# Kernel optimization log

Hardware: AMD Instinct MI355X
Metric: run time of the kernel (lower is better)

## Reference

```python
import jax, jax.numpy as jnp
import numpy as np

B, O, M, H, E = 32, 64, 128, 4, 64  # batch, num_obj, memory_len, heads, embed


def setup_inputs() -> dict:
    key = jax.random.key(0)
    ks = jax.random.split(key, 10)
    s = 1.0 / np.sqrt(E)
    return {
        "query": jax.random.normal(ks[0], (B, O, E), jnp.float32),
        "context": jax.random.normal(ks[1], (B, M, E), jnp.float32),
        "memory": jax.random.normal(ks[2], (B, M, E), jnp.float32),
        "W_ch": jax.random.normal(ks[3], (E, H * E), jnp.float32) * s,
        "b_ch": jax.random.normal(ks[4], (H * E,), jnp.float32) * s,
        "w_logit": jax.random.normal(ks[5], (E,), jnp.float32) * s,
        "b_logit": jax.random.normal(ks[6], (1,), jnp.float32) * s,
        "W_rh": jax.random.normal(ks[7], (H * E, E), jnp.float32) * (1.0 / np.sqrt(H * E)),
        "b_rh": jax.random.normal(ks[8], (E,), jnp.float32) * (1.0 / np.sqrt(H * E)),
        "temp": jnp.float32(1.0),
    }


def reference(query, context, memory, W_ch, b_ch, w_logit, b_logit, W_rh, b_rh, temp):
    # create heads: [B,O,E] -> [B,O,H,E]
    q = (query @ W_ch + b_ch).reshape(B, O, H, E)
    # broadcast add query heads and context over memory axis: [B,O,M,H,E]
    qc = jnp.tanh(context[:, None, :, None, :] + q[:, :, None, :, :])
    # logit projection -> [B,O,M,H]
    logits = jnp.einsum("bomhe,e->bomh", qc, w_logit) + b_logit[0]
    # softmax over memory axis (dim=2)
    probs = jax.nn.softmax(logits / temp, axis=2)
    # weighted sum of memory over M: [B,O,H,E]
    heads = jnp.einsum("bomh,bme->bohe", probs, memory)
    heads = jax.nn.leaky_relu(heads, negative_slope=0.01)
    out = heads.reshape(B, O, H * E) @ W_rh + b_rh
    return out
```

## Files before the change

### kernel.cpp

```cpp
#include <hip/hip_runtime.h>
#include <hip/hip_fp16.h>

#define B 32
#define O 64
#define M 128
#define H 4
#define E 64
#define SC 2.88539008177792681f
#define LOG2E 1.44269504088896341f

#if __has_builtin(__builtin_amdgcn_exp2f)
#define EXP2F(x) __builtin_amdgcn_exp2f(x)
#else
#define EXP2F(x) __exp2f(x)
#endif

__device__ __forceinline__ float rl(float v, int lane) {
    return __uint_as_float(__builtin_amdgcn_readlane(__float_as_uint(v), lane));
}
__device__ __forceinline__ unsigned pk2h(float a, float b) {
    return (unsigned)__half_as_ushort(__float2half_rn(a)) |
           ((unsigned)__half_as_ushort(__float2half_rn(b)) << 16);
}

__global__ __launch_bounds__(256) void prep_kernel(
    const float* __restrict__ query, const float* __restrict__ context,
    const float* __restrict__ memory, const float* __restrict__ W_ch,
    const float* __restrict__ b_ch,
    __half* __restrict__ ctx_Eh, __half* __restrict__ mem_T, float* __restrict__ q_E)
{
    __shared__ float s[128 * 68];
    const int t = threadIdx.x, blk = blockIdx.x;

    if (blk < 64) {
        const int b = blk & 31;
        const bool is_ctx = blk < 32;
        const int e = t >> 2, mb = (t & 3) * 32;
        const float* src = (is_ctx ? context : memory) + b * (M * E);
        #pragma unroll
        for (int i = 0; i < 8; ++i) {
            int idx = i * 1024 + t * 4;
            float4 v = *(const float4*)(src + idx);
            *(float4*)(&s[(idx >> 6) * 68 + (idx & 63)]) = v;
        }
        __syncthreads();
        if (is_ctx) {
            uint4* dst = (uint4*)(ctx_Eh + (size_t)b * (E * M) + e * M + mb);
            #pragma unroll
            for (int qd = 0; qd < 4; ++qd) {
                unsigned u[4];
                #pragma unroll
                for (int k = 0; k < 4; ++k) {
                    int m0 = mb + qd * 8 + 2 * k;
                    float ea = fminf(EXP2F(SC * s[m0 * 68 + e]), 60000.f);
                    float eb = fminf(EXP2F(SC * s[(m0 + 1) * 68 + e]), 60000.f);
                    u[k] = pk2h(ea, eb);
                }
                dst[qd] = make_uint4(u[0], u[1], u[2], u[3]);
            }
        } else {
            uint4* dst = (uint4*)(mem_T + (size_t)b * (E * M) + e * M + mb);
            #pragma unroll
            for (int qd = 0; qd < 4; ++qd) {
                unsigned u[4];
                #pragma unroll
                for (int k = 0; k < 4; ++k) {
                    int m0 = mb + qd * 8 + 2 * k;
                    u[k] = pk2h(s[m0 * 68 + e], s[(m0 + 1) * 68 + e]);
                }
                dst[qd] = make_uint4(u[0], u[1], u[2], u[3]);
            }
        }
    } else {
        const int r0 = (blk - 64) * 4;
        s[t] = query[(r0 + (t & 3)) * 64 + (t >> 2)];
        __syncthreads();
        float bc = b_ch[t];
        float a0 = bc, a1 = bc, a2 = bc, a3 = bc;
        #pragma unroll 8
        for (int k = 0; k < 64; ++k) {
            float4 qv = *(const float4*)(&s[k * 4]);
            float wv = W_ch[k * 256 + t];
            a0 = fmaf(qv.x, wv, a0);
            a1 = fmaf(qv.y, wv, a1);
            a2 = fmaf(qv.z, wv, a2);
            a3 = fmaf(qv.w, wv, a3);
        }
        float* qa = q_E + (size_t)r0 * 256 + t;
        qa[0]   = EXP2F(SC * a0);
        qa[256] = EXP2F(SC * a1);
        qa[512] = EXP2F(SC * a2);
        qa[768] = EXP2F(SC * a3);
    }
}

__global__ __launch_bounds__(256) void attn_main(
    const __half* __restrict__ ctx_Eh, const __half* __restrict__ mem_T,
    const float* __restrict__ q_E, const float* __restrict__ w_logit,
    const float* __restrict__ b_logit, const float* __restrict__ temp,
    const float* __restrict__ W_rh, const float* __restrict__ b_rh,
    float* __restrict__ out)
{
    __shared__ __half s_E[E * M];
    __shared__ float4 s_qwu[H * E];
    __shared__ float  s_prob0[M * H];
    __shared__ float  s_prob1[M * H];
    __shared__ float  s_part0[H * 4 * E];
    __shared__ float  s_part1[H * 4 * E];
    __shared__ float  s_po0[4 * E];
    __shared__ float  s_po1[4 * E];

    const int t = threadIdx.x, lane = t & 63, w = t >> 6;
    const int bo0 = blockIdx.x * 2, bo1 = bo0 + 1, b = bo0 >> 6;

    {
        const uint4* g = (const uint4*)(ctx_Eh + (size_t)b * (E * M));
        uint4* l = (uint4*)s_E;
        #pragma unroll
        for (int p = 0; p < 4; ++p)
            l[p * 256 + t] = g[p * 256 + t];
    }
    const float wl = w_logit[lane];
    s_qwu[t] = make_float4(wl, q_E[bo0 * 256 + t], q_E[bo1 * 256 + t], 0.f);
    float sumw = wl;
    #pragma unroll
    for (int sft = 1; sft < 64; sft <<= 1) sumw += __shfl_xor(sumw, sft);
    const float bl   = b_logit[0];
    const float lsc  = LOG2E / temp[0];
    const float base = (sumw + bl) * lsc;
    const float lsc2 = -2.0f * lsc;
    __syncthreads();

    float a00 = 0.f, a01 = 0.f, a10 = 0.f, a11 = 0.f;
    const __half2* Ep = (const __half2*)s_E;
    const float4*  qp = &s_qwu[w * 64];
    #pragma unroll 4
    for (int e = 0; e < 64; ++e) {
        float2 cf = __half22float2(Ep[e * 64 + lane]);
        float4 qw = qp[e];
        float t00 = fmaf(cf.x, qw.y, 1.0f);
        float t01 = fmaf(cf.y, qw.y, 1.0f);
        float t10 = fmaf(cf.x, qw.z, 1.0f);
        float t11 = fmaf(cf.y, qw.z, 1.0f);
        float r0 = __builtin_amdgcn_rcpf(t00 * t01);
        float r1 = __builtin_amdgcn_rcpf(t10 * t11);
        float w0 = qw.x * r0;
        float w1 = qw.x * r1;
        a00 = fmaf(w0, t01, a00);  a01 = fmaf(w0, t00, a01);
        a10 = fmaf(w1, t11, a10);  a11 = fmaf(w1, t10, a11);
    }

    uint4 mr[4];
    {
        const uint4* mp = (const uint4*)(mem_T + (size_t)b * (E * M) + lane * M + 32 * w);
        mr[0] = mp[0]; mr[1] = mp[1]; mr[2] = mp[2]; mr[3] = mp[3];
    }

    float l00 = fmaf(lsc2, a00, base), l01 = fmaf(lsc2, a01, base);
    float l10 = fmaf(lsc2, a10, base), l11 = fmaf(lsc2, a11, base);
    float mx0 = fmaxf(l00, l01), mx1 = fmaxf(l10, l11);
    #pragma unroll
    for (int sft = 1; sft < 64; sft <<= 1) {
        mx0 = fmaxf(mx0, __shfl_xor(mx0, sft));
        mx1 = fmaxf(mx1, __shfl_xor(mx1, sft));
    }
    float e00 = EXP2F(l00 - mx0), e01 = EXP2F(l01 - mx0);
    float e10 = EXP2F(l10 - mx1), e11 = EXP2F(l11 - mx1);
    float s0 = e00 + e01, s1 = e10 + e11;
    #pragma unroll
    for (int sft = 1; sft < 64; sft <<= 1) {
        s0 += __shfl_xor(s0, sft);
        s1 += __shfl_xor(s1, sft);
    }
    float rs0 = __builtin_amdgcn_rcpf(s0), rs1 = __builtin_amdgcn_rcpf(s1);
    s_prob0[(2 * lane) * H + w]     = e00 * rs0;
    s_prob0[(2 * lane + 1) * H + w] = e01 * rs0;
    s_prob1[(2 * lane) * H + w]     = e10 * rs1;
    s_prob1[(2 * lane + 1) * H + w] = e11 * rs1;
    __syncthreads();

    float h00 = 0.f, h01 = 0.f, h02 = 0.f, h03 = 0.f;
    float h10 = 0.f, h11 = 0.f, h12 = 0.f, h13 = 0.f;
    {
        union { uint4 u4[4]; __half2 h2[16]; } mu;
        mu.u4[0] = mr[0]; mu.u4[1] = mr[1]; mu.u4[2] = mr[2]; mu.u4[3] = mr[3];
        const int mbase = 32 * w;
        #pragma unroll 8
        for (int j = 0; j < 16; ++j) {
            float2 mv = __half22float2(mu.h2[j]);
            int m = mbase + 2 * j;
            float4 pa = *(const float4*)(&s_prob0[m * 4]);
            float4 pb = *(const float4*)(&s_prob0[(m + 1) * 4]);
            h00 = fmaf(pa.x, mv.x, h00); h01 = fmaf(pa.y, mv.x, h01);
            h02 = fmaf(pa.z, mv.x, h02); h03 = fmaf(pa.w, mv.x, h03);
            h00 = fmaf(pb.x, mv.y, h00); h01 = fmaf(pb.y, mv.y, h01);
            h02 = fmaf(pb.z, mv.y, h02); h03 = fmaf(pb.w, mv.y, h03);
            float4 pc = *(const float4*)(&s_prob1[m * 4]);
            float4 pd = *(const float4*)(&s_prob1[(m + 1) * 4]);
            h10 = fmaf(pc.x, mv.x, h10); h11 = fmaf(pc.y, mv.x, h11);
            h12 = fmaf(pc.z, mv.x, h12); h13 = fmaf(pc.w, mv.x, h13);
            h10 = fmaf(pd.x, mv.y, h10); h11 = fmaf(pd.y, mv.y, h11);
            h12 = fmaf(pd.z, mv.y, h12); h13 = fmaf(pd.w, mv.y, h13);
        }
    }
    s_part0[0 * 256 + w * 64 + lane] = h00;
    s_part0[1 * 256 + w * 64 + lane] = h01;
    s_part0[2 * 256 + w * 64 + lane] = h02;
    s_part0[3 * 256 + w * 64 + lane] = h03;
    s_part1[0 * 256 + w * 64 + lane] = h10;
    s_part1[1 * 256 + w * 64 + lane] = h11;
    s_part1[2 * 256 + w * 64 + lane] = h12;
    s_part1[3 * 256 + w * 64 + lane] = h13;
    __syncthreads();
    float hv0 = s_part0[w * 256 + lane] + s_part0[w * 256 + 64 + lane]
              + s_part0[w * 256 + 128 + lane] + s_part0[w * 256 + 192 + lane];
    float hv1 = s_part1[w * 256 + lane] + s_part1[w * 256 + 64 + lane]
              + s_part1[w * 256 + 128 + lane] + s_part1[w * 256 + 192 + lane];
    hv0 = (hv0 > 0.f) ? hv0 : 0.01f * hv0;
    hv1 = (hv1 > 0.f) ? hv1 : 0.01f * hv1;

    {
        float acc0 = 0.f, acc1 = 0.f;
        const float* Wp = W_rh + (w * 64) * 64 + lane;
        #pragma unroll 8
        for (int jj = 0; jj < 64; ++jj) {
            float wv = Wp[jj * 64];
            float hj0 = rl(hv0, jj);
            float hj1 = rl(hv1, jj);
            acc0 = fmaf(hj0, wv, acc0);
            acc1 = fmaf(hj1, wv, acc1);
        }
        s_po0[w * 64 + lane] = acc0;
        s_po1[w * 64 + lane] = acc1;
    }
    __syncthreads();
    if (t < 64) {
        float o = s_po0[t] + s_po0[64 + t] + s_po0[128 + t] + s_po0[192 + t] + b_rh[t];
        out[(size_t)bo0 * 64 + t] = o;
    } else if (t < 128) {
        int e2 = t - 64;
        float o = s_po1[e2] + s_po1[64 + e2] + s_po1[128 + e2] + s_po1[192 + e2] + b_rh[e2];
        out[(size_t)bo1 * 64 + e2] = o;
    }
}

extern "C" void kernel_launch(void* const* d_in, const int* in_sizes, int n_in,
                              void* d_out, int out_size, void* d_ws, size_t ws_size,
                              hipStream_t stream) {
    const float* query   = (const float*)d_in[0];
    const float* context = (const float*)d_in[1];
    const float* memory  = (const float*)d_in[2];
    const float* W_ch    = (const float*)d_in[3];
    const float* b_ch    = (const float*)d_in[4];
    const float* w_logit = (const float*)d_in[5];
    const float* b_logit = (const float*)d_in[6];
    const float* W_rh    = (const float*)d_in[7];
    const float* b_rh    = (const float*)d_in[8];
    const float* temp    = (const float*)d_in[9];
    float* out = (float*)d_out;

    __half* ctx_Eh  = (__half*)d_ws;
    __half* mem_T   = ctx_Eh + (size_t)B * E * M;
    float*  q_E     = (float*)(mem_T + (size_t)B * E * M);

    prep_kernel<<<576, 256, 0, stream>>>(query, context, memory, W_ch, b_ch,
                                         ctx_Eh, mem_T, q_E);
    attn_main<<<B * O / 2, 256, 0, stream>>>(ctx_Eh, mem_T, q_E, w_logit,
                                             b_logit, temp, W_rh, b_rh, out);
}
```

Baseline: 99.16 us.

## Keep per-head softmax and weighted sum in-wave using readlane broadcasts

Each wave now works on its own head end to end. The query and logit weights are broadcast with readlane instead of being staged as float4 in shared memory, and the probability-weighted memory sum is computed inside the wave, reading probabilities through readlane. The memory tile is staged in LDS as packed half2 words with a padded stride. This removes the cross-wave probability and partial-sum exchanges and two barriers, but adds many scalar readlane operations and strided LDS reads.

Result: no change. 99.81 us (+0.6%).

```diff
diff --git a/kernel.cpp b/kernel.cpp
--- a/kernel.cpp
+++ b/kernel.cpp
@@ -8,6 +8,7 @@
 #define E 64
 #define SC 2.88539008177792681f
 #define LOG2E 1.44269504088896341f
+#define MSTR 65
 
 #if __has_builtin(__builtin_amdgcn_exp2f)
 #define EXP2F(x) __builtin_amdgcn_exp2f(x)
@@ -102,11 +103,7 @@
     float* __restrict__ out)
 {
     __shared__ __half s_E[E * M];
-    __shared__ float4 s_qwu[H * E];
-    __shared__ float  s_prob0[M * H];
-    __shared__ float  s_prob1[M * H];
-    __shared__ float  s_part0[H * 4 * E];
-    __shared__ float  s_part1[H * 4 * E];
+    __shared__ float  s_M[E * MSTR];
     __shared__ float  s_po0[4 * E];
     __shared__ float  s_po1[4 * E];
 
@@ -120,8 +117,19 @@
         for (int p = 0; p < 4; ++p)
             l[p * 256 + t] = g[p * 256 + t];
     }
-    const float wl = w_logit[lane];
-    s_qwu[t] = make_float4(wl, q_E[bo0 * 256 + t], q_E[bo1 * 256 + t], 0.f);
+    {
+        const uint2* g = (const uint2*)(mem_T + (size_t)b * (E * M));
+        const int e = t >> 2, j0 = (t & 3) * 16;
+        #pragma unroll
+        for (int i = 0; i < 8; ++i) {
+            uint2 v = g[e * 32 + (j0 >> 1) + i];
+            s_M[e * MSTR + j0 + 2 * i]     = __uint_as_float(v.x);
+            s_M[e * MSTR + j0 + 2 * i + 1] = __uint_as_float(v.y);
+        }
+    }
+    const float wl  = w_logit[lane];
+    const float qE0 = q_E[bo0 * 256 + t];
+    const float qE1 = q_E[bo1 * 256 + t];
     float sumw = wl;
     #pragma unroll
     for (int sft = 1; sft < 64; sft <<= 1) sumw += __shfl_xor(sumw, sft);
@@ -133,27 +141,22 @@
 
     float a00 = 0.f, a01 = 0.f, a10 = 0.f, a11 = 0.f;
     const __half2* Ep = (const __half2*)s_E;
-    const float4*  qp = &s_qwu[w * 64];
     #pragma unroll 4
     for (int e = 0; e < 64; ++e) {
         float2 cf = __half22float2(Ep[e * 64 + lane]);
-        float4 qw = qp[e];
-        float t00 = fmaf(cf.x, qw.y, 1.0f);
-        float t01 = fmaf(cf.y, qw.y, 1.0f);
-        float t10 = fmaf(cf.x, qw.z, 1.0f);
-        float t11 = fmaf(cf.y, qw.z, 1.0f);
+        float q0 = rl(qE0, e);
+        float q1 = rl(qE1, e);
+        float we = rl(wl, e);
+        float t00 = fmaf(cf.x, q0, 1.0f);
+        float t01 = fmaf(cf.y, q0, 1.0f);
+        float t10 = fmaf(cf.x, q1, 1.0f);
+        float t11 = fmaf(cf.y, q1, 1.0f);
         float r0 = __builtin_amdgcn_rcpf(t00 * t01);
         float r1 = __builtin_amdgcn_rcpf(t10 * t11);
-        float w0 = qw.x * r0;
-        float w1 = qw.x * r1;
+        float w0 = we * r0;
+        float w1 = we * r1;
         a00 = fmaf(w0, t01, a00);  a01 = fmaf(w0, t00, a01);
         a10 = fmaf(w1, t11, a10);  a11 = fmaf(w1, t10, a11);
-    }
-
-    uint4 mr[4];
-    {
-        const uint4* mp = (const uint4*)(mem_T + (size_t)b * (E * M) + lane * M + 32 * w);
-        mr[0] = mp[0]; mr[1] = mp[1]; mr[2] = mp[2]; mr[3] = mp[3];
     }
 
     float l00 = fmaf(lsc2, a00, base), l01 = fmaf(lsc2, a01, base);
@@ -173,49 +176,22 @@
         s1 += __shfl_xor(s1, sft);
     }
     float rs0 = __builtin_amdgcn_rcpf(s0), rs1 = __builtin_amdgcn_rcpf(s1);
-    s_prob0[(2 * lane) * H + w]     = e00 * rs0;
-    s_prob0[(2 * lane + 1) * H + w] = e01 * rs0;
-    s_prob1[(2 * lane) * H + w]     = e10 * rs1;
-    s_prob1[(2 * lane + 1) * H + w] = e11 * rs1;
-    __syncthreads();
-
-    float h00 = 0.f, h01 = 0.f, h02 = 0.f, h03 = 0.f;
-    float h10 = 0.f, h11 = 0.f, h12 = 0.f, h13 = 0.f;
-    {
-        union { uint4 u4[4]; __half2 h2[16]; } mu;
-        mu.u4[0] = mr[0]; mu.u4[1] = mr[1]; mu.u4[2] = mr[2]; mu.u4[3] = mr[3];
-        const int mbase = 32 * w;
+
+    float h0 = 0.f, h1 = 0.f;
+    {
+        const float* mrow = &s_M[lane * MSTR];
         #pragma unroll 8
-        for (int j = 0; j < 16; ++j) {
-            float2 mv = __half22float2(mu.h2[j]);
-            int m = mbase + 2 * j;
-            float4 pa = *(const float4*)(&s_prob0[m * 4]);
-            float4 pb = *(const float4*)(&s_prob0[(m + 1) * 4]);
-            h00 = fmaf(pa.x, mv.x, h00); h01 = fmaf(pa.y, mv.x, h01);
-            h02 = fmaf(pa.z, mv.x, h02); h03 = fmaf(pa.w, mv.x, h03);
-            h00 = fmaf(pb.x, mv.y, h00); h01 = fmaf(pb.y, mv.y, h01);
-            h02 = fmaf(pb.z, mv.y, h02); h03 = fmaf(pb.w, mv.y, h03);
-            float4 pc = *(const float4*)(&s_prob1[m * 4]);
-            float4 pd = *(const float4*)(&s_prob1[(m + 1) * 4]);
-            h10 = fmaf(pc.x, mv.x, h10); h11 = fmaf(pc.y, mv.x, h11);
-            h12 = fmaf(pc.z, mv.x, h12); h13 = fmaf(pc.w, mv.x, h13);
-            h10 = fmaf(pd.x, mv.y, h10); h11 = fmaf(pd.y, mv.y, h11);
-            h12 = fmaf(pd.z, mv.y, h12); h13 = fmaf(pd.w, mv.y, h13);
-        }
-    }
-    s_part0[0 * 256 + w * 64 + lane] = h00;
-    s_part0[1 * 256 + w * 64 + lane] = h01;
-    s_part0[2 * 256 + w * 64 + lane] = h02;
-    s_part0[3 * 256 + w * 64 + lane] = h03;
-    s_part1[0 * 256 + w * 64 + lane] = h10;
-    s_part1[1 * 256 + w * 64 + lane] = h11;
-    s_part1[2 * 256 + w * 64 + lane] = h12;
-    s_part1[3 * 256 + w * 64 + lane] = h13;
-    __syncthreads();
-    float hv0 = s_part0[w * 256 + lane] + s_part0[w * 256 + 64 + lane]
-              + s_part0[w * 256 + 128 + lane] + s_part0[w * 256 + 192 + lane];
-    float hv1 = s_part1[w * 256 + lane] + s_part1[w * 256 + 64 + lane]
-              + s_part1[w * 256 + 128 + lane] + s_part1[w * 256 + 192 + lane];
+        for (int j = 0; j < 64; ++j) {
+            __half2 mh = *(const __half2*)&mrow[j];
+            float2 mv = __half22float2(mh);
+            float p00 = rl(e00, j), p01 = rl(e01, j);
+            float p10 = rl(e10, j), p11 = rl(e11, j);
+            h0 = fmaf(p00, mv.x, h0); h0 = fmaf(p01, mv.y, h0);
+            h1 = fmaf(p10, mv.x, h1); h1 = fmaf(p11, mv.y, h1);
+        }
+    }
+    float hv0 = h0 * rs0;
+    float hv1 = h1 * rs1;
     hv0 = (hv0 > 0.f) ? hv0 : 0.01f * hv0;
     hv1 = (hv1 > 0.f) ? hv1 : 0.01f * hv1;
 
@@ -225,10 +201,8 @@
         #pragma unroll 8
         for (int jj = 0; jj < 64; ++jj) {
             float wv = Wp[jj * 64];
-            float hj0 = rl(hv0, jj);
-            float hj1 = rl(hv1, jj);
-            acc0 = fmaf(hj0, wv, acc0);
-            acc1 = fmaf(hj1, wv, acc1);
+            acc0 = fmaf(rl(hv0, jj), wv, acc0);
+            acc1 = fmaf(rl(hv1, jj), wv, acc1);
         }
         s_po0[w * 64 + lane] = acc0;
         s_po1[w * 64 + lane] = acc1;
```
